# Performance work log

Hardware: AMD Instinct MI355X
Metric: run time of the kernel (lower is better)

## Reference

```python
import jax, jax.numpy as jnp
import numpy as np

B, T, K, FT, FP, N, H, HEADS, C = 8, 5, 20, 384, 3, 128, 64, 8, 2
ALPHA = 0.2
NEG = -9e15


def gru(x, Wi, Wh, bi, bh):
    # x: [M, L, F] -> (full [M, L, Hd], last [M, Hd]); torch nn.GRU cell math
    Hd = Wh.shape[0]
    gx = jnp.einsum('mlf,fg->mlg', x, Wi) + bi  # precompute input projections

    def step(h, gxt):
        gh = h @ Wh + bh
        xr, xz, xn = jnp.split(gxt, 3, axis=-1)
        hr, hz, hn = jnp.split(gh, 3, axis=-1)
        r = jax.nn.sigmoid(xr + hr)
        z = jax.nn.sigmoid(xz + hz)
        n = jnp.tanh(xn + r * hn)
        h = (1. - z) * n + z * h
        return h, h

    h0 = jnp.zeros((x.shape[0], Hd), x.dtype)
    last, full = jax.lax.scan(step, h0, jnp.swapaxes(gx, 0, 1))
    return jnp.swapaxes(full, 0, 1), last


def temporal_attn(full, last):
    # attend over time using the last hidden state as the query
    a = jax.nn.softmax(jnp.einsum('mlh,mh->ml', full, last), axis=-1)
    return jnp.einsum('ml,mlh->mh', a, full)


def gat_forward(s, p, adj, sm1_Wi, sm1_Wh, sm1_bi, sm1_bh,
                sm2_Wi, sm2_Wh, sm2_bi, sm2_bh,
                pr_Wi, pr_Wh, pr_bi, pr_bh,
                Wb, bb, Wx, bx, W1, a1, W2, a2):
    mask = adj > 0  # [N, N]
    # --- SMEncoder: vectorized over (batch, stock, day) ---
    s_ = jnp.transpose(s, (0, 4, 1, 2, 3)).reshape(B * N * T, K, FT)
    f1, l1 = gru(s_, sm1_Wi, sm1_Wh, sm1_bi, sm1_bh)
    cv = temporal_attn(f1, l1).reshape(B * N, T, H)          # intra-day context
    f2, l2 = gru(cv, sm2_Wi, sm2_Wh, sm2_bi, sm2_bh)
    ct = temporal_attn(f2, l2).reshape(B, N, H)              # inter-day context
    # --- PriceEncoder: vectorized over (batch, stock) ---
    p_ = jnp.transpose(p, (0, 3, 1, 2)).reshape(B * N, T, FP)
    f3, l3 = gru(p_, pr_Wi, pr_Wh, pr_bi, pr_bh)
    qt = temporal_attn(f3, l3).reshape(B, N, H)
    # --- bilinear fusion + per-stock linear head (dropout is eval-mode identity) ---
    X = jnp.tanh(jnp.einsum('bni,oij,bnj->bno', ct, Wb, qt) + bb)   # [B, N, H]
    out1 = jnp.tanh(jnp.einsum('bnh,nch->bnc', X, Wx) + bx)          # [B, N, C]
    # --- multi-head GAT layer 1 (concat + LeakyReLU + adj-masked softmax) ---
    Whd = jnp.einsum('bnh,khf->bknf', X, W1)                         # [B, heads, N, H]
    e = jax.nn.leaky_relu(
        jnp.einsum('bknf,kf->bkn', Whd, a1[:, :H])[:, :, :, None]
        + jnp.einsum('bknf,kf->bkn', Whd, a1[:, H:])[:, :, None, :], ALPHA)
    att = jax.nn.softmax(jnp.where(mask, e, NEG), axis=-1)
    Xh = jax.nn.elu(jnp.einsum('bknm,bkmf->bknf', att, Whd))
    X2 = jnp.transpose(Xh, (0, 2, 1, 3)).reshape(B, N, HEADS * H)    # head concat
    # --- GAT layer 2 -> num_classes ---
    Wh2 = X2 @ W2                                                    # [B, N, C]
    e2 = jax.nn.leaky_relu((Wh2 @ a2[:C])[:, :, None]
                           + (Wh2 @ a2[C:])[:, None, :], ALPHA)
    att2 = jax.nn.softmax(jnp.where(mask, e2, NEG), axis=-1)
    Xo = jnp.einsum('bnm,bmc->bnc', att2, Wh2)
    return jnp.transpose(Xo + out1, (0, 2, 1))                       # [B, C, N]


def setup_inputs():
    key = jax.random.key(0)
    ks = jax.random.split(key, 23)
    g = lambda k, sh, sc=0.05: jax.random.normal(k, sh, jnp.float32) * sc
    adj = (jax.random.uniform(ks[2], (N, N)) < 0.3).astype(jnp.float32)
    adj = jnp.maximum(adj, jnp.eye(N, dtype=jnp.float32))
    return {
        's': jax.random.normal(ks[0], (B, T, K, FT, N), jnp.float32),
        'p': jax.random.normal(ks[1], (B, T, FP, N), jnp.float32),
        'adj': adj,
        'sm1_Wi': g(ks[3], (FT, 3 * H)), 'sm1_Wh': g(ks[4], (H, 3 * H)),
        'sm1_bi': g(ks[5], (3 * H,)), 'sm1_bh': g(ks[6], (3 * H,)),
        'sm2_Wi': g(ks[7], (H, 3 * H)), 'sm2_Wh': g(ks[8], (H, 3 * H)),
        'sm2_bi': g(ks[9], (3 * H,)), 'sm2_bh': g(ks[10], (3 * H,)),
        'pr_Wi': g(ks[11], (FP, 3 * H)), 'pr_Wh': g(ks[12], (H, 3 * H)),
        'pr_bi': g(ks[13], (3 * H,)), 'pr_bh': g(ks[14], (3 * H,)),
        'Wb': g(ks[15], (H, H, H)), 'bb': g(ks[16], (H,)),
        'Wx': g(ks[17], (N, C, H)), 'bx': g(ks[18], (N, C)),
        'W1': g(ks[19], (HEADS, H, H)), 'a1': g(ks[20], (HEADS, 2 * H)),
        'W2': g(ks[21], (HEADS * H, C)), 'a2': g(ks[22], (2 * C,)),
    }


def reference(s, p, adj, sm1_Wi, sm1_Wh, sm1_bi, sm1_bh,
              sm2_Wi, sm2_Wh, sm2_bi, sm2_bh,
              pr_Wi, pr_Wh, pr_bi, pr_bh,
              Wb, bb, Wx, bx, W1, a1, W2, a2):
    return gat_forward(s, p, adj, sm1_Wi, sm1_Wh, sm1_bi, sm1_bh,
                       sm2_Wi, sm2_Wh, sm2_bi, sm2_bh,
                       pr_Wi, pr_Wh, pr_bi, pr_bh,
                       Wb, bb, Wx, bx, W1, a1, W2, a2)
```

## Files before the change

### kernel.cpp

```cpp
#include <hip/hip_runtime.h>
#include <hip/hip_bf16.h>
#include <hip/hip_fp16.h>

#define DI __device__ __forceinline__

namespace {

constexpr int G_  = 192;
constexpr int FT_ = 384;

typedef _Float16 f16x8 __attribute__((ext_vector_type(8)));
typedef _Float16 f16x4 __attribute__((ext_vector_type(4)));
typedef float    f32x4 __attribute__((ext_vector_type(4)));

DI float rcpf(float x) { return __builtin_amdgcn_rcpf(x); }
DI float lrelu(float x) { return x > 0.f ? x : 0.2f * x; }
DI float sigmoidf(float x) { return rcpf(1.f + __expf(-x)); }
DI float tanh_fast(float x) { return 1.f - 2.f * rcpf(__expf(2.f * x) + 1.f); }

__global__ __launch_bounds__(256) void k_cvtB(
    const float* __restrict__ Wi, _Float16* __restrict__ Bt) {
  int v = blockIdx.x * 256 + threadIdx.x;
  int g = v / 384, f = v % 384;
  Bt[v] = (_Float16)Wi[f * 192 + g];
}

__global__ __launch_bounds__(256) void k_gx1(
    const float* __restrict__ s, const _Float16* __restrict__ Bt,
    const float* __restrict__ bi, _Float16* __restrict__ gx1) {
  const int slab = blockIdx.x;
  const int b = slab / 100, rem = slab % 100, t = rem / 20, k = rem % 20;
  const float* A = s + (size_t)((b * 5 + t) * 20 + k) * (FT_ * 128);
  __shared__ __align__(16) _Float16 AsL[128 * 40];
  __shared__ __align__(16) _Float16 BsL[192 * 40];
  __shared__ __align__(16) float bisL[192];
  const int tid = threadIdx.x;
  if (tid < 192) bisL[tid] = bi[tid];
  const int w = tid >> 6, l = tid & 63;
  const int lr = l & 15, lk = l >> 4;

  f32x4 acc[12][2];
#pragma unroll
  for (int gt = 0; gt < 12; ++gt)
#pragma unroll
    for (int nt = 0; nt < 2; ++nt) acc[gt][nt] = (f32x4){0.f, 0.f, 0.f, 0.f};

  for (int kc = 0; kc < 12; ++kc) {
    const int f0 = kc * 32;
#pragma unroll
    for (int pass = 0; pass < 2; ++pass) {
      int task = tid + 256 * pass;
      int n = task & 127, oct = task >> 7;
      const float* src = A + (size_t)(f0 + oct * 8) * 128 + n;
      float v[8];
#pragma unroll
      for (int j = 0; j < 8; ++j) v[j] = src[j * 128];
      f16x8 h;
#pragma unroll
      for (int j = 0; j < 8; ++j) h[j] = (_Float16)v[j];
      *(f16x8*)&AsL[n * 40 + oct * 8] = h;
    }
#pragma unroll
    for (int pass = 0; pass < 3; ++pass) {
      int c = tid + 256 * pass;
      int g = c >> 2, oct = c & 3;
      f16x8 h = *(const f16x8*)&Bt[(size_t)g * 384 + f0 + oct * 8];
      *(f16x8*)&BsL[g * 40 + oct * 8] = h;
    }
    __syncthreads();
    f16x8 aN[2];
#pragma unroll
    for (int nt = 0; nt < 2; ++nt)
      aN[nt] = *(const f16x8*)&AsL[(w * 32 + nt * 16 + lr) * 40 + lk * 8];
#pragma unroll
    for (int gt = 0; gt < 12; ++gt) {
      f16x8 bW = *(const f16x8*)&BsL[(gt * 16 + lr) * 40 + lk * 8];
      acc[gt][0] = __builtin_amdgcn_mfma_f32_16x16x32_f16(bW, aN[0], acc[gt][0], 0, 0, 0);
      acc[gt][1] = __builtin_amdgcn_mfma_f32_16x16x32_f16(bW, aN[1], acc[gt][1], 0, 0, 0);
    }
    __syncthreads();
  }
  const size_t base3 = ((size_t)k * 40 + b * 5 + t) * 8;
#pragma unroll
  for (int nt = 0; nt < 2; ++nt) {
    const int ngrp = w * 2 + nt;
    _Float16* dstbase = gx1 + ((base3 + ngrp) * 3) * 1024 + (size_t)l * 16;
#pragma unroll
    for (int gate = 0; gate < 3; ++gate) {
      f16x8 h0, h1;
#pragma unroll
      for (int tq = 0; tq < 4; ++tq) {
        const int gt = gate * 4 + tq;
        f32x4 bias = *(const f32x4*)&bisL[gt * 16 + lk * 4];
        f32x4 c = acc[gt][nt];
#pragma unroll
        for (int r = 0; r < 4; ++r) {
          float v = c[r] + bias[r];
          if (tq < 2) h0[tq * 4 + r] = (_Float16)v;
          else        h1[(tq - 2) * 4 + r] = (_Float16)v;
        }
      }
      *(f16x8*)(dstbase + (size_t)gate * 1024) = h0;
      *(f16x8*)(dstbase + (size_t)gate * 1024 + 8) = h1;
    }
  }
}

__global__ __launch_bounds__(64, 1) void k_scan1m(
    const _Float16* __restrict__ gx, const float* __restrict__ Wh,
    const float* __restrict__ bh, _Float16* __restrict__ cvh) {
  const int wv = blockIdx.x;
  const int b = wv / 40, rem = wv % 40, t = rem / 8, ng = rem % 8;
  const int l = threadIdx.x;
  const int seq = l & 15, rg = l >> 4;

  __shared__ __align__(16) _Float16 histL[20][64][24];
  __shared__ __align__(16) _Float16 red[16][72];

  f16x8 whF[12][2];
#pragma unroll
  for (int gt = 0; gt < 12; ++gt)
#pragma unroll
    for (int c = 0; c < 2; ++c) {
      f16x8 h;
#pragma unroll
      for (int j = 0; j < 8; ++j)
        h[j] = (_Float16)Wh[(size_t)(32 * c + rg * 8 + j) * 192 + gt * 16 + seq];
      whF[gt][c] = h;
    }
  f32x4 bhF[12];
#pragma unroll
  for (int gt = 0; gt < 12; ++gt)
    bhF[gt] = *(const f32x4*)&bh[gt * 16 + rg * 4];

  float h16[16];
#pragma unroll
  for (int j = 0; j < 16; ++j) h16[j] = 0.f;

#define GXP(kk) (gx + ((((size_t)(kk) * 40 + b * 5 + t) * 8 + ng) * 3) * 1024 + (size_t)l * 16)

  f16x8 gxc[3][2], gxn[3][2], gxn2[3][2];
  {
    const _Float16* p0 = GXP(0);
    const _Float16* p1 = GXP(1);
    const _Float16* p2 = GXP(2);
#pragma unroll
    for (int g = 0; g < 3; ++g) {
      gxc[g][0]  = *(const f16x8*)(p0 + g * 1024);
      gxc[g][1]  = *(const f16x8*)(p0 + g * 1024 + 8);
      gxn[g][0]  = *(const f16x8*)(p1 + g * 1024);
      gxn[g][1]  = *(const f16x8*)(p1 + g * 1024 + 8);
      gxn2[g][0] = *(const f16x8*)(p2 + g * 1024);
      gxn2[g][1] = *(const f16x8*)(p2 + g * 1024 + 8);
    }
  }

  f16x8 bf0, bf1;
  f32x4 acc[12];

#define GATES_AND_H(KCONST_HIST)                                               \
  {                                                                            \
    _Float16* hp = &histL[KCONST_HIST][l][0];                                  \
    f16x8 p0, p1;                                                              \
    _Pragma("unroll")                                                          \
    for (int tq = 0; tq < 4; ++tq) {                                           \
      _Pragma("unroll")                                                        \
      for (int r = 0; r < 4; ++r) {                                            \
        const int idx = tq * 4 + r;                                            \
        float xr = (float)gxc[0][idx >> 3][idx & 7];                           \
        float xz = (float)gxc[1][idx >> 3][idx & 7];                           \
        float xn = (float)gxc[2][idx >> 3][idx & 7];                           \
        float hr = acc[tq][r], hz = acc[4 + tq][r], hnv = acc[8 + tq][r];      \
        float rr = sigmoidf(xr + hr);                                          \
        float zz = sigmoidf(xz + hz);                                          \
        float nn = tanh_fast(xn + rr * hnv);                                   \
        float hv = (1.f - zz) * nn + zz * h16[idx];                            \
        h16[idx] = hv;                                                         \
        if (idx < 8) p0[idx] = (_Float16)hv; else p1[idx - 8] = (_Float16)hv;  \
      }                                                                        \
    }                                                                          \
    *(f16x8*)hp = p0;                                                          \
    *(f16x8*)(hp + 8) = p1;                                                    \
  }

#define REDIST()                                                               \
  {                                                                            \
    _Pragma("unroll")                                                          \
    for (int tq = 0; tq < 4; ++tq) {                                           \
      f16x4 q;                                                                 \
      q[0] = (_Float16)h16[tq * 4 + 0]; q[1] = (_Float16)h16[tq * 4 + 1];      \
      q[2] = (_Float16)h16[tq * 4 + 2]; q[3] = (_Float16)h16[tq * 4 + 3];      \
      *(f16x4*)&red[seq][16 * tq + 4 * rg] = q;                                \
    }                                                                          \
    bf0 = *(const f16x8*)&red[seq][8 * rg];                                    \
    bf1 = *(const f16x8*)&red[seq][32 + 8 * rg];                               \
  }

#pragma unroll
  for (int gt = 0; gt < 12; ++gt) acc[gt] = bhF[gt];
  GATES_AND_H(0)
  REDIST()

  for (int k = 1; k < 19; ++k) {
#pragma unroll
    for (int g = 0; g < 3; ++g) {
      gxc[g][0] = gxn[g][0];  gxc[g][1] = gxn[g][1];
      gxn[g][0] = gxn2[g][0]; gxn[g][1] = gxn2[g][1];
    }
    if (k < 18) {
      const _Float16* pn = GXP(k + 2);
#pragma unroll
      for (int g = 0; g < 3; ++g) {
        gxn2[g][0] = *(const f16x8*)(pn + g * 1024);
        gxn2[g][1] = *(const f16x8*)(pn + g * 1024 + 8);
      }
    }
#pragma unroll
    for (int gt = 0; gt < 12; ++gt) {
      acc[gt] = bhF[gt];
      acc[gt] = __builtin_amdgcn_mfma_f32_16x16x32_f16(whF[gt][0], bf0, acc[gt], 0, 0, 0);
      acc[gt] = __builtin_amdgcn_mfma_f32_16x16x32_f16(whF[gt][1], bf1, acc[gt], 0, 0, 0);
    }
    GATES_AND_H(k)
    REDIST()
  }

#pragma unroll
  for (int g = 0; g < 3; ++g) { gxc[g][0] = gxn[g][0]; gxc[g][1] = gxn[g][1]; }
#pragma unroll
  for (int gt = 0; gt < 12; ++gt) {
    acc[gt] = bhF[gt];
    acc[gt] = __builtin_amdgcn_mfma_f32_16x16x32_f16(whF[gt][0], bf0, acc[gt], 0, 0, 0);
    acc[gt] = __builtin_amdgcn_mfma_f32_16x16x32_f16(whF[gt][1], bf1, acc[gt], 0, 0, 0);
  }
  GATES_AND_H(19)

  float d[20];
#pragma unroll
  for (int kk = 0; kk < 20; ++kk) {
    f16x8 a0 = *(const f16x8*)&histL[kk][l][0];
    f16x8 a1 = *(const f16x8*)&histL[kk][l][8];
    float p = 0.f;
#pragma unroll
    for (int j = 0; j < 8; ++j)
      p += (float)a0[j] * h16[j] + (float)a1[j] * h16[8 + j];
    p += __shfl_xor(p, 16);
    p += __shfl_xor(p, 32);
    d[kk] = p;
  }
  float mx = d[0];
#pragma unroll
  for (int kk = 1; kk < 20; ++kk) mx = fmaxf(mx, d[kk]);
  float sum = 0.f;
#pragma unroll
  for (int kk = 0; kk < 20; ++kk) { d[kk] = __expf(d[kk] - mx); sum += d[kk]; }
  const float inv = rcpf(sum);
  float av[16];
#pragma unroll
  for (int j = 0; j < 16; ++j) av[j] = 0.f;
#pragma unroll
  for (int kk = 0; kk < 20; ++kk) {
    f16x8 a0 = *(const f16x8*)&histL[kk][l][0];
    f16x8 a1 = *(const f16x8*)&histL[kk][l][8];
    float wgt = d[kk] * inv;
#pragma unroll
    for (int j = 0; j < 8; ++j) {
      av[j]     += wgt * (float)a0[j];
      av[8 + j] += wgt * (float)a1[j];
    }
  }
  const int n = ng * 16 + seq;
  const size_t seqg = (size_t)b * 128 + n;
  _Float16* dst = cvh + (seqg * 5 + t) * 64;
#pragma unroll
  for (int tq = 0; tq < 4; ++tq) {
    f16x4 q;
    q[0] = (_Float16)av[tq * 4 + 0]; q[1] = (_Float16)av[tq * 4 + 1];
    q[2] = (_Float16)av[tq * 4 + 2]; q[3] = (_Float16)av[tq * 4 + 3];
    *(f16x4*)&dst[16 * tq + 4 * rg] = q;
  }
#undef GXP
#undef GATES_AND_H
#undef REDIST
}

__global__ __launch_bounds__(64, 1) void k_scan2m(
    const _Float16* __restrict__ cvh, const float* __restrict__ Wi,
    const float* __restrict__ Wh, const float* __restrict__ bi,
    const float* __restrict__ bh, float* __restrict__ ct) {
  const int l = threadIdx.x;
  const int seq = l & 15, rg = l >> 4;
  const size_t seqg0 = (size_t)blockIdx.x * 16;

  __shared__ __align__(16) _Float16 histL[5][64][24];
  __shared__ __align__(16) _Float16 red[16][72];

  f16x8 wiF[12][2], whF[12][2];
#pragma unroll
  for (int gt = 0; gt < 12; ++gt)
#pragma unroll
    for (int c = 0; c < 2; ++c) {
      f16x8 hi, hh;
#pragma unroll
      for (int j = 0; j < 8; ++j) {
        hi[j] = (_Float16)Wi[(size_t)(32 * c + rg * 8 + j) * 192 + gt * 16 + seq];
        hh[j] = (_Float16)Wh[(size_t)(32 * c + rg * 8 + j) * 192 + gt * 16 + seq];
      }
      wiF[gt][c] = hi; whF[gt][c] = hh;
    }
  f32x4 biF[12], bhF[12];
#pragma unroll
  for (int gt = 0; gt < 12; ++gt) {
    biF[gt] = *(const f32x4*)&bi[gt * 16 + rg * 4];
    bhF[gt] = *(const f32x4*)&bh[gt * 16 + rg * 4];
  }

  float h16[16];
#pragma unroll
  for (int j = 0; j < 16; ++j) h16[j] = 0.f;
  f16x8 bf0, bf1;

#pragma unroll
  for (int t = 0; t < 5; ++t) {
    const _Float16* xp = cvh + ((seqg0 + seq) * 5 + t) * 64;
    f16x8 xf0 = *(const f16x8*)(xp + 8 * rg);
    f16x8 xf1 = *(const f16x8*)(xp + 32 + 8 * rg);
    f32x4 accX[12], accH[12];
#pragma unroll
    for (int gt = 0; gt < 12; ++gt) {
      accX[gt] = biF[gt];
      accX[gt] = __builtin_amdgcn_mfma_f32_16x16x32_f16(wiF[gt][0], xf0, accX[gt], 0, 0, 0);
      accX[gt] = __builtin_amdgcn_mfma_f32_16x16x32_f16(wiF[gt][1], xf1, accX[gt], 0, 0, 0);
      accH[gt] = bhF[gt];
      if (t > 0) {
        accH[gt] = __builtin_amdgcn_mfma_f32_16x16x32_f16(whF[gt][0], bf0, accH[gt], 0, 0, 0);
        accH[gt] = __builtin_amdgcn_mfma_f32_16x16x32_f16(whF[gt][1], bf1, accH[gt], 0, 0, 0);
      }
    }
    _Float16* hp = &histL[t][l][0];
    f16x8 p0, p1;
#pragma unroll
    for (int tq = 0; tq < 4; ++tq) {
#pragma unroll
      for (int r = 0; r < 4; ++r) {
        const int idx = tq * 4 + r;
        float xr = accX[tq][r], xz = accX[4 + tq][r], xn = accX[8 + tq][r];
        float hr = accH[tq][r], hz = accH[4 + tq][r], hnv = accH[8 + tq][r];
        float rr = sigmoidf(xr + hr);
        float zz = sigmoidf(xz + hz);
        float nn = tanh_fast(xn + rr * hnv);
        float hv = (1.f - zz) * nn + zz * h16[idx];
        h16[idx] = hv;
        if (idx < 8) p0[idx] = (_Float16)hv; else p1[idx - 8] = (_Float16)hv;
      }
    }
    *(f16x8*)hp = p0;
    *(f16x8*)(hp + 8) = p1;
    if (t < 4) {
#pragma unroll
      for (int tq = 0; tq < 4; ++tq) {
        f16x4 q;
        q[0] = (_Float16)h16[tq * 4 + 0]; q[1] = (_Float16)h16[tq * 4 + 1];
        q[2] = (_Float16)h16[tq * 4 + 2]; q[3] = (_Float16)h16[tq * 4 + 3];
        *(f16x4*)&red[seq][16 * tq + 4 * rg] = q;
      }
      bf0 = *(const f16x8*)&red[seq][8 * rg];
      bf1 = *(const f16x8*)&red[seq][32 + 8 * rg];
    }
  }

  float d[5];
#pragma unroll
  for (int kk = 0; kk < 5; ++kk) {
    f16x8 a0 = *(const f16x8*)&histL[kk][l][0];
    f16x8 a1 = *(const f16x8*)&histL[kk][l][8];
    float p = 0.f;
#pragma unroll
    for (int j = 0; j < 8; ++j)
      p += (float)a0[j] * h16[j] + (float)a1[j] * h16[8 + j];
    p += __shfl_xor(p, 16);
    p += __shfl_xor(p, 32);
    d[kk] = p;
  }
  float mx = d[0];
#pragma unroll
  for (int kk = 1; kk < 5; ++kk) mx = fmaxf(mx, d[kk]);
  float sum = 0.f;
#pragma unroll
  for (int kk = 0; kk < 5; ++kk) { d[kk] = __expf(d[kk] - mx); sum += d[kk]; }
  const float inv = rcpf(sum);
  float av[16];
#pragma unroll
  for (int j = 0; j < 16; ++j) av[j] = 0.f;
#pragma unroll
  for (int kk = 0; kk < 5; ++kk) {
    f16x8 a0 = *(const f16x8*)&histL[kk][l][0];
    f16x8 a1 = *(const f16x8*)&histL[kk][l][8];
    float wgt = d[kk] * inv;
#pragma unroll
    for (int j = 0; j < 8; ++j) {
      av[j]     += wgt * (float)a0[j];
      av[8 + j] += wgt * (float)a1[j];
    }
  }
  float* dst = ct + (seqg0 + seq) * 64;
#pragma unroll
  for (int tq = 0; tq < 4; ++tq) {
    float4 o = make_float4(av[tq * 4], av[tq * 4 + 1], av[tq * 4 + 2], av[tq * 4 + 3]);
    *(float4*)&dst[16 * tq + 4 * rg] = o;
  }
}

__global__ __launch_bounds__(192) void k_scan3(
    const float* __restrict__ p, const float* __restrict__ Wi,
    const float* __restrict__ Wh, const float* __restrict__ bi,
    const float* __restrict__ bh, float* __restrict__ outv) {
  const int s0 = blockIdx.x * 4;
  const int tid = threadIdx.x;
  __shared__ __align__(16) float hist[4][5][64];
  __shared__ float xp[4][3];
  __shared__ float ghl[4][192], gxl[4][192];
  __shared__ float dls[4][5], als[4][5];
  float wic[3], whc[64];
#pragma unroll
  for (int f = 0; f < 3; ++f) wic[f] = Wi[f * G_ + tid];
#pragma unroll
  for (int i = 0; i < 64; ++i) whc[i] = Wh[i * G_ + tid];
  const float big = bi[tid], bhg = bh[tid];

  for (int t = 0; t < 5; ++t) {
    if (tid < 12) {
      int ss = tid / 3, f = tid % 3;
      int seq = s0 + ss, b = seq >> 7, n = seq & 127;
      xp[ss][f] = p[((size_t)(b * 5 + t) * 3 + f) * 128 + n];
    }
    __syncthreads();
#pragma unroll
    for (int ss = 0; ss < 4; ++ss) {
      gxl[ss][tid] = xp[ss][0] * wic[0] + xp[ss][1] * wic[1] + xp[ss][2] * wic[2] + big;
      float ah = 0.f;
      if (t > 0) {
        const float4* hq = (const float4*)&hist[ss][t - 1][0];
#pragma unroll
        for (int q = 0; q < 16; ++q) {
          float4 h4 = hq[q];
          ah += h4.x * whc[4 * q]     + h4.y * whc[4 * q + 1]
              + h4.z * whc[4 * q + 2] + h4.w * whc[4 * q + 3];
        }
      }
      ghl[ss][tid] = ah + bhg;
    }
    __syncthreads();
#pragma unroll
    for (int base = 0; base < 256; base += 192) {
      int tk = base + tid;
      if (tk < 256) {
        int ss = tk >> 6, i = tk & 63;
        float xr = gxl[ss][i], xz = gxl[ss][64 + i], xn = gxl[ss][128 + i];
        float hr = ghl[ss][i], hz = ghl[ss][64 + i], hn = ghl[ss][128 + i];
        float r  = sigmoidf(xr + hr);
        float z  = sigmoidf(xz + hz);
        float nn = tanh_fast(xn + r * hn);
        float hp = (t == 0) ? 0.f : hist[ss][t - 1][i];
        hist[ss][t][i] = (1.f - z) * nn + z * hp;
      }
    }
    __syncthreads();
  }
  if (tid < 20) {
    int ss = tid / 5, kk = tid % 5;
    float d = 0.f;
#pragma unroll
    for (int i = 0; i < 64; ++i) d += hist[ss][kk][i] * hist[ss][4][i];
    dls[ss][kk] = d;
  }
  __syncthreads();
  if (tid < 20) {
    int ss = tid / 5, kk = tid % 5;
    float mx = -3.4e38f;
#pragma unroll
    for (int j = 0; j < 5; ++j) mx = fmaxf(mx, dls[ss][j]);
    als[ss][kk] = __expf(dls[ss][kk] - mx);
  }
  __syncthreads();
  for (int idx = tid; idx < 256; idx += 192) {
    int ss = idx >> 6, i = idx & 63;
    float sum = 0.f, a = 0.f;
#pragma unroll
    for (int kk = 0; kk < 5; ++kk) sum += als[ss][kk];
#pragma unroll
    for (int kk = 0; kk < 5; ++kk) a += als[ss][kk] * hist[ss][kk][i];
    outv[(size_t)(s0 + ss) * 64 + i] = a * rcpf(sum);
  }
}

__global__ __launch_bounds__(256) void k_bilinear(
    const float* __restrict__ ct, const float* __restrict__ qt,
    const float* __restrict__ Wb, const float* __restrict__ bb,
    float* __restrict__ X) {
  const int bn0 = blockIdx.x * 4;
  const int tid = threadIdx.x;
  __shared__ float ctl[4][64], qtl[4][64];
  {
    int ss = tid >> 6, i = tid & 63;
    ctl[ss][i] = ct[(size_t)(bn0 + ss) * 64 + i];
    qtl[ss][i] = qt[(size_t)(bn0 + ss) * 64 + i];
  }
  __syncthreads();
  const int o = tid >> 2, part = tid & 3, j0 = part << 4;
  float qr[4][16];
#pragma unroll
  for (int pp = 0; pp < 4; ++pp)
#pragma unroll
    for (int q = 0; q < 16; ++q) qr[pp][q] = qtl[pp][j0 + q];
  float acc[4] = {0.f, 0.f, 0.f, 0.f};
  const float* wb = Wb + (size_t)o * 4096 + j0;
  for (int i = 0; i < 64; ++i) {
    const float4* w4 = (const float4*)(wb + i * 64);
    float tmp[4] = {0.f, 0.f, 0.f, 0.f};
#pragma unroll
    for (int q = 0; q < 4; ++q) {
      float4 w = w4[q];
#pragma unroll
      for (int pp = 0; pp < 4; ++pp)
        tmp[pp] += w.x * qr[pp][4 * q]     + w.y * qr[pp][4 * q + 1]
                 + w.z * qr[pp][4 * q + 2] + w.w * qr[pp][4 * q + 3];
    }
#pragma unroll
    for (int pp = 0; pp < 4; ++pp) acc[pp] += ctl[pp][i] * tmp[pp];
  }
#pragma unroll
  for (int pp = 0; pp < 4; ++pp) {
    acc[pp] += __shfl_xor(acc[pp], 1);
    acc[pp] += __shfl_xor(acc[pp], 2);
  }
  if (part == 0) {
    float bbv = bb[o];
#pragma unroll
    for (int pp = 0; pp < 4; ++pp)
      X[(size_t)(bn0 + pp) * 64 + o] = tanh_fast(acc[pp] + bbv);
  }
}

__global__ __launch_bounds__(256) void k_gat1(
    const float* __restrict__ X, const float* __restrict__ W1,
    const float* __restrict__ a1, const float* __restrict__ adj,
    float* __restrict__ X2) {
  const int bid = blockIdx.x;
  const int b = bid >> 4, k = (bid >> 1) & 7, nh = bid & 1;
  const int tid = threadIdx.x;
  __shared__ __align__(16) float whd[128][68];
  __shared__ float w1l[64][64];
  __shared__ float d1l[128], d2l[128];
  for (int v = tid; v < 4096; v += 256) w1l[v >> 6][v & 63] = W1[(size_t)k * 4096 + v];
  __syncthreads();
  {
    const int f = tid & 63, ng = tid >> 6;
    const float* Xb = X + (size_t)b * 128 * 64;
    for (int n = ng * 32; n < ng * 32 + 32; ++n) {
      float a = 0.f;
#pragma unroll
      for (int h = 0; h < 64; ++h) a += Xb[n * 64 + h] * w1l[h][f];
      whd[n][f] = a;
    }
  }
  __syncthreads();
  if (tid < 128) {
    const int n = tid;
    float da = 0.f, db = 0.f;
#pragma unroll
    for (int f = 0; f < 64; ++f) {
      float w = whd[n][f];
      da += w * a1[k * 128 + f];
      db += w * a1[k * 128 + 64 + f];
    }
    d1l[n] = da; d2l[n] = db;
  }
  __syncthreads();
  {
    const int n = nh * 64 + (tid & 63), fq = tid >> 6, f0 = fq * 16;
    unsigned long long mlo = 0ull, mhi = 0ull;
    for (int m = 0; m < 64; ++m) if (adj[n * 128 + m] > 0.f)      mlo |= (1ull << m);
    for (int m = 0; m < 64; ++m) if (adj[n * 128 + 64 + m] > 0.f) mhi |= (1ull << m);
    const float d1n = d1l[n];
    float mx = -3.4e38f;
    for (int m = 0; m < 128; ++m) {
      bool on = (m < 64) ? (((mlo >> m) & 1ull) != 0) : (((mhi >> (m - 64)) & 1ull) != 0);
      float e = lrelu(d1n + d2l[m]);
      mx = fmaxf(mx, on ? e : -3.4e38f);
    }
    float sum = 0.f;
    float acc[16];
#pragma unroll
    for (int q = 0; q < 16; ++q) acc[q] = 0.f;
    for (int m = 0; m < 128; ++m) {
      bool on = (m < 64) ? (((mlo >> m) & 1ull) != 0) : (((mhi >> (m - 64)) & 1ull) != 0);
      float w = on ? __expf(lrelu(d1n + d2l[m]) - mx) : 0.f;
      sum += w;
      const float4* wr = (const float4*)&whd[m][f0];
#pragma unroll
      for (int q4 = 0; q4 < 4; ++q4) {
        float4 wv = wr[q4];
        acc[4 * q4]     += w * wv.x;
        acc[4 * q4 + 1] += w * wv.y;
        acc[4 * q4 + 2] += w * wv.z;
        acc[4 * q4 + 3] += w * wv.w;
      }
    }
    float inv = rcpf(sum);
    float* dst = X2 + ((size_t)b * 128 + n) * 512 + k * 64 + f0;
#pragma unroll
    for (int q = 0; q < 16; ++q) {
      float v = acc[q] * inv;
      dst[q] = v > 0.f ? v : (__expf(v) - 1.f);
    }
  }
}

__global__ __launch_bounds__(256) void k_wh2(
    const float* __restrict__ X, const float* __restrict__ Wx, const float* __restrict__ bx,
    const float* __restrict__ X2, const float* __restrict__ W2, const float* __restrict__ a2,
    float* __restrict__ out1g, float* __restrict__ wh2g,
    float* __restrict__ d2ag, float* __restrict__ d2bg) {
  const int b = blockIdx.x >> 3, nq = blockIdx.x & 7;
  const int tid = threadIdx.x;
  __shared__ float w2l[1024];
  for (int v = tid; v < 1024; v += 256) w2l[v] = W2[v];
  __syncthreads();
  const int w = tid >> 6, l = tid & 63;
  const float a20 = a2[0], a21 = a2[1], a22 = a2[2], a23 = a2[3];
#pragma unroll
  for (int it = 0; it < 4; ++it) {
    int n = nq * 16 + w * 4 + it;
    int bn = b * 128 + n;
    const float* xr = X2 + (size_t)bn * 512 + l * 8;
    float4 xa = *(const float4*)xr;
    float4 xb = *(const float4*)(xr + 4);
    float xs[8] = {xa.x, xa.y, xa.z, xa.w, xb.x, xb.y, xb.z, xb.w};
    float s0 = 0.f, s1 = 0.f;
#pragma unroll
    for (int j = 0; j < 8; ++j) {
      s0 += xs[j] * w2l[(l * 8 + j) * 2];
      s1 += xs[j] * w2l[(l * 8 + j) * 2 + 1];
    }
#pragma unroll
    for (int d = 1; d < 64; d <<= 1) { s0 += __shfl_xor(s0, d); s1 += __shfl_xor(s1, d); }
    if (l == 0) {
      wh2g[bn * 2] = s0; wh2g[bn * 2 + 1] = s1;
      d2ag[bn] = s0 * a20 + s1 * a21;
      d2bg[bn] = s0 * a22 + s1 * a23;
    }
  }
  if (tid < 32) {
    int n = nq * 16 + (tid >> 1), c = tid & 1;
    int bn = b * 128 + n;
    const float* xrow = X + (size_t)bn * 64;
    float a = 0.f;
#pragma unroll
    for (int h = 0; h < 64; ++h) a += xrow[h] * Wx[(n * 2 + c) * 64 + h];
    out1g[bn * 2 + c] = tanh_fast(a + bx[n * 2 + c]);
  }
}

__global__ __launch_bounds__(128) void k_final(
    const float* __restrict__ adj, const float* __restrict__ wh2g,
    const float* __restrict__ d2ag, const float* __restrict__ d2bg,
    const float* __restrict__ out1g, float* __restrict__ out) {
  const int b = blockIdx.x;
  const int tid = threadIdx.x;
  __shared__ float wh2l[128][2];
  __shared__ float dbl_[128];
  wh2l[tid][0] = wh2g[(size_t)(b * 128 + tid) * 2];
  wh2l[tid][1] = wh2g[(size_t)(b * 128 + tid) * 2 + 1];
  dbl_[tid] = d2bg[b * 128 + tid];
  __syncthreads();
  const int n = tid;
  unsigned long long mlo = 0ull, mhi = 0ull;
  for (int m = 0; m < 64; ++m) if (adj[n * 128 + m] > 0.f)      mlo |= (1ull << m);
  for (int m = 0; m < 64; ++m) if (adj[n * 128 + 64 + m] > 0.f) mhi |= (1ull << m);
  const float dan = d2ag[b * 128 + n];
  float mx = -3.4e38f;
  for (int m = 0; m < 128; ++m) {
    bool on = (m < 64) ? (((mlo >> m) & 1ull) != 0) : (((mhi >> (m - 64)) & 1ull) != 0);
    float e = lrelu(dan + dbl_[m]);
    mx = fmaxf(mx, on ? e : -3.4e38f);
  }
  float sum = 0.f, x0 = 0.f, x1 = 0.f;
  for (int m = 0; m < 128; ++m) {
    bool on = (m < 64) ? (((mlo >> m) & 1ull) != 0) : (((mhi >> (m - 64)) & 1ull) != 0);
    float w = on ? __expf(lrelu(dan + dbl_[m]) - mx) : 0.f;
    sum += w; x0 += w * wh2l[m][0]; x1 += w * wh2l[m][1];
  }
  float inv = rcpf(sum);
  out[(size_t)(b * 2 + 0) * 128 + n] = x0 * inv + out1g[(size_t)(b * 128 + n) * 2];
  out[(size_t)(b * 2 + 1) * 128 + n] = x1 * inv + out1g[(size_t)(b * 128 + n) * 2 + 1];
}

}

extern "C" void kernel_launch(void* const* d_in, const int* in_sizes, int n_in,
                              void* d_out, int out_size, void* d_ws, size_t ws_size,
                              hipStream_t stream) {
  (void)in_sizes; (void)n_in; (void)out_size;
  const float* s      = (const float*)d_in[0];
  const float* p      = (const float*)d_in[1];
  const float* adj    = (const float*)d_in[2];
  const float* sm1_Wi = (const float*)d_in[3];
  const float* sm1_Wh = (const float*)d_in[4];
  const float* sm1_bi = (const float*)d_in[5];
  const float* sm1_bh = (const float*)d_in[6];
  const float* sm2_Wi = (const float*)d_in[7];
  const float* sm2_Wh = (const float*)d_in[8];
  const float* sm2_bi = (const float*)d_in[9];
  const float* sm2_bh = (const float*)d_in[10];
  const float* pr_Wi  = (const float*)d_in[11];
  const float* pr_Wh  = (const float*)d_in[12];
  const float* pr_bi  = (const float*)d_in[13];
  const float* pr_bh  = (const float*)d_in[14];
  const float* Wb     = (const float*)d_in[15];
  const float* bb     = (const float*)d_in[16];
  const float* Wx     = (const float*)d_in[17];
  const float* bx     = (const float*)d_in[18];
  const float* W1     = (const float*)d_in[19];
  const float* a1     = (const float*)d_in[20];
  const float* W2     = (const float*)d_in[21];
  const float* a2     = (const float*)d_in[22];

  if (ws_size < 43540480u) return;
  char* ws = (char*)d_ws;
  _Float16* gx1  = (_Float16*)ws;
  _Float16* cvh  = (_Float16*)(ws + 39321600);
  float* ct      = (float*)(ws + 40632320);
  float* qt      = (float*)(ws + 40894464);
  float* X       = (float*)(ws + 41156608);
  float* X2      = (float*)(ws + 41418752);
  _Float16* Bt   = (_Float16*)(ws + 41418752);
  float* wh2g    = (float*)(ws + 43515904);
  float* out1g   = (float*)(ws + 43524096);
  float* d2ag    = (float*)(ws + 43532288);
  float* d2bg    = (float*)(ws + 43536384);

  hipLaunchKernelGGL(k_cvtB,     dim3(288),  dim3(256), 0, stream, sm1_Wi, Bt);
  hipLaunchKernelGGL(k_gx1,      dim3(800),  dim3(256), 0, stream, s, Bt, sm1_bi, gx1);
  hipLaunchKernelGGL(k_scan1m,   dim3(320),  dim3(64),  0, stream, gx1, sm1_Wh, sm1_bh, cvh);
  hipLaunchKernelGGL(k_scan2m,   dim3(64),   dim3(64),  0, stream, cvh, sm2_Wi, sm2_Wh, sm2_bi, sm2_bh, ct);
  hipLaunchKernelGGL(k_scan3,    dim3(256),  dim3(192), 0, stream, p, pr_Wi, pr_Wh, pr_bi, pr_bh, qt);
  hipLaunchKernelGGL(k_bilinear, dim3(256),  dim3(256), 0, stream, ct, qt, Wb, bb, X);
  hipLaunchKernelGGL(k_gat1,     dim3(128),  dim3(256), 0, stream, X, W1, a1, adj, X2);
  hipLaunchKernelGGL(k_wh2,      dim3(64),   dim3(256), 0, stream, X, Wx, bx, X2, W2, a2, out1g, wh2g, d2ag, d2bg);
  hipLaunchKernelGGL(k_final,    dim3(8),    dim3(128), 0, stream, adj, wh2g, d2ag, d2bg, out1g, (float*)d_out);
}
```

Measured before the change: 476.5 us.

## Merge price GRU into MFMA scan2 kernel and fuse GAT head kernels

The price-encoder GRU now runs inside the scan2 MFMA kernel as an extra 64 blocks, computing its tiny input projection with scalar FMAs from shared memory and its recurrence with the same MFMA path. The separate scalar k_scan3 kernel is removed. The k_wh2 and k_final kernels are merged into one per-batch k_head kernel that keeps intermediates in shared memory, which saves a launch and the global round trips. The trade-off is that the head now uses only 8 blocks for the W2 projection work, so it has less parallelism, and the price GRU now uses fp16 MFMA inputs instead of fp32.

```diff
diff --git a/kernel.cpp b/kernel.cpp
--- a/kernel.cpp
+++ b/kernel.cpp
@@ -284,35 +284,68 @@
 #undef REDIST
 }
 
-__global__ __launch_bounds__(64, 1) void k_scan2m(
-    const _Float16* __restrict__ cvh, const float* __restrict__ Wi,
-    const float* __restrict__ Wh, const float* __restrict__ bi,
-    const float* __restrict__ bh, float* __restrict__ ct) {
+__global__ __launch_bounds__(64, 1) void k_scan23(
+    const _Float16* __restrict__ cvh, const float* __restrict__ Wi2,
+    const float* __restrict__ Wh2w, const float* __restrict__ bi2,
+    const float* __restrict__ bh2, float* __restrict__ ct,
+    const float* __restrict__ p, const float* __restrict__ Wi3,
+    const float* __restrict__ Wh3, const float* __restrict__ bi3,
+    const float* __restrict__ bh3, float* __restrict__ qt) {
   const int l = threadIdx.x;
   const int seq = l & 15, rg = l >> 4;
-  const size_t seqg0 = (size_t)blockIdx.x * 16;
 
   __shared__ __align__(16) _Float16 histL[5][64][24];
   __shared__ __align__(16) _Float16 red[16][72];
-
-  f16x8 wiF[12][2], whF[12][2];
+  __shared__ float wi3L[576];
+  __shared__ float bi3L[192];
+  __shared__ float x3L[240];
+
+  const bool isPrice = blockIdx.x >= 64;
+  const size_t seqg0 = (size_t)(isPrice ? blockIdx.x - 64 : blockIdx.x) * 16;
+  const float* Wh = isPrice ? Wh3 : Wh2w;
+  const float* bh = isPrice ? bh3 : bh2;
+
+  f16x8 whF[12][2];
 #pragma unroll
   for (int gt = 0; gt < 12; ++gt)
 #pragma unroll
     for (int c = 0; c < 2; ++c) {
-      f16x8 hi, hh;
-#pragma unroll
-      for (int j = 0; j < 8; ++j) {
-        hi[j] = (_Float16)Wi[(size_t)(32 * c + rg * 8 + j) * 192 + gt * 16 + seq];
+      f16x8 hh;
+#pragma unroll
+      for (int j = 0; j < 8; ++j)
         hh[j] = (_Float16)Wh[(size_t)(32 * c + rg * 8 + j) * 192 + gt * 16 + seq];
+      whF[gt][c] = hh;
+    }
+  f32x4 bhF[12];
+#pragma unroll
+  for (int gt = 0; gt < 12; ++gt)
+    bhF[gt] = *(const f32x4*)&bh[gt * 16 + rg * 4];
+
+  f16x8 wiF[12][2];
+  f32x4 biF[12];
+  if (!isPrice) {
+#pragma unroll
+    for (int gt = 0; gt < 12; ++gt)
+#pragma unroll
+      for (int c = 0; c < 2; ++c) {
+        f16x8 hi;
+#pragma unroll
+        for (int j = 0; j < 8; ++j)
+          hi[j] = (_Float16)Wi2[(size_t)(32 * c + rg * 8 + j) * 192 + gt * 16 + seq];
+        wiF[gt][c] = hi;
       }
-      wiF[gt][c] = hi; whF[gt][c] = hh;
-    }
-  f32x4 biF[12], bhF[12];
-#pragma unroll
-  for (int gt = 0; gt < 12; ++gt) {
-    biF[gt] = *(const f32x4*)&bi[gt * 16 + rg * 4];
-    bhF[gt] = *(const f32x4*)&bh[gt * 16 + rg * 4];
+#pragma unroll
+    for (int gt = 0; gt < 12; ++gt)
+      biF[gt] = *(const f32x4*)&bi2[gt * 16 + rg * 4];
+  } else {
+    const int b = (int)(seqg0 >> 7), n0 = (int)(seqg0 & 127);
+    for (int idx = l; idx < 576; idx += 64) wi3L[idx] = Wi3[idx];
+    for (int idx = l; idx < 192; idx += 64) bi3L[idx] = bi3[idx];
+    for (int idx = l; idx < 240; idx += 64) {
+      int t = idx / 48, r = idx % 48, f = r / 16, sq = r % 16;
+      x3L[idx] = p[((size_t)(b * 5 + t) * 3 + f) * 128 + n0 + sq];
+    }
+    __syncthreads();
   }
 
   float h16[16];
@@ -322,15 +355,36 @@
 
 #pragma unroll
   for (int t = 0; t < 5; ++t) {
-    const _Float16* xp = cvh + ((seqg0 + seq) * 5 + t) * 64;
-    f16x8 xf0 = *(const f16x8*)(xp + 8 * rg);
-    f16x8 xf1 = *(const f16x8*)(xp + 32 + 8 * rg);
     f32x4 accX[12], accH[12];
+    if (!isPrice) {
+      const _Float16* xp = cvh + ((seqg0 + seq) * 5 + t) * 64;
+      f16x8 xf0 = *(const f16x8*)(xp + 8 * rg);
+      f16x8 xf1 = *(const f16x8*)(xp + 32 + 8 * rg);
+#pragma unroll
+      for (int gt = 0; gt < 12; ++gt) {
+        accX[gt] = biF[gt];
+        accX[gt] = __builtin_amdgcn_mfma_f32_16x16x32_f16(wiF[gt][0], xf0, accX[gt], 0, 0, 0);
+        accX[gt] = __builtin_amdgcn_mfma_f32_16x16x32_f16(wiF[gt][1], xf1, accX[gt], 0, 0, 0);
+      }
+    } else {
+      const float x0 = x3L[t * 48 + seq];
+      const float x1 = x3L[t * 48 + 16 + seq];
+      const float x2 = x3L[t * 48 + 32 + seq];
+#pragma unroll
+      for (int G = 0; G < 3; ++G)
+#pragma unroll
+        for (int tq = 0; tq < 4; ++tq) {
+          f32x4 v;
+#pragma unroll
+          for (int r = 0; r < 4; ++r) {
+            const int g = G * 64 + 16 * tq + 4 * rg + r;
+            v[r] = bi3L[g] + wi3L[g] * x0 + wi3L[192 + g] * x1 + wi3L[384 + g] * x2;
+          }
+          accX[G * 4 + tq] = v;
+        }
+    }
 #pragma unroll
     for (int gt = 0; gt < 12; ++gt) {
-      accX[gt] = biF[gt];
-      accX[gt] = __builtin_amdgcn_mfma_f32_16x16x32_f16(wiF[gt][0], xf0, accX[gt], 0, 0, 0);
-      accX[gt] = __builtin_amdgcn_mfma_f32_16x16x32_f16(wiF[gt][1], xf1, accX[gt], 0, 0, 0);
       accH[gt] = bhF[gt];
       if (t > 0) {
         accH[gt] = __builtin_amdgcn_mfma_f32_16x16x32_f16(whF[gt][0], bf0, accH[gt], 0, 0, 0);
@@ -374,13 +428,13 @@
   for (int kk = 0; kk < 5; ++kk) {
     f16x8 a0 = *(const f16x8*)&histL[kk][l][0];
     f16x8 a1 = *(const f16x8*)&histL[kk][l][8];
-    float p = 0.f;
+    float pq = 0.f;
 #pragma unroll
     for (int j = 0; j < 8; ++j)
-      p += (float)a0[j] * h16[j] + (float)a1[j] * h16[8 + j];
-    p += __shfl_xor(p, 16);
-    p += __shfl_xor(p, 32);
-    d[kk] = p;
+      pq += (float)a0[j] * h16[j] + (float)a1[j] * h16[8 + j];
+    pq += __shfl_xor(pq, 16);
+    pq += __shfl_xor(pq, 32);
+    d[kk] = pq;
   }
   float mx = d[0];
 #pragma unroll
@@ -403,94 +457,11 @@
       av[8 + j] += wgt * (float)a1[j];
     }
   }
-  float* dst = ct + (seqg0 + seq) * 64;
+  float* dst = (isPrice ? qt : ct) + (seqg0 + seq) * 64;
 #pragma unroll
   for (int tq = 0; tq < 4; ++tq) {
     float4 o = make_float4(av[tq * 4], av[tq * 4 + 1], av[tq * 4 + 2], av[tq * 4 + 3]);
     *(float4*)&dst[16 * tq + 4 * rg] = o;
-  }
-}
-
-__global__ __launch_bounds__(192) void k_scan3(
-    const float* __restrict__ p, const float* __restrict__ Wi,
-    const float* __restrict__ Wh, const float* __restrict__ bi,
-    const float* __restrict__ bh, float* __restrict__ outv) {
-  const int s0 = blockIdx.x * 4;
-  const int tid = threadIdx.x;
-  __shared__ __align__(16) float hist[4][5][64];
-  __shared__ float xp[4][3];
-  __shared__ float ghl[4][192], gxl[4][192];
-  __shared__ float dls[4][5], als[4][5];
-  float wic[3], whc[64];
-#pragma unroll
-  for (int f = 0; f < 3; ++f) wic[f] = Wi[f * G_ + tid];
-#pragma unroll
-  for (int i = 0; i < 64; ++i) whc[i] = Wh[i * G_ + tid];
-  const float big = bi[tid], bhg = bh[tid];
-
-  for (int t = 0; t < 5; ++t) {
-    if (tid < 12) {
-      int ss = tid / 3, f = tid % 3;
-      int seq = s0 + ss, b = seq >> 7, n = seq & 127;
-      xp[ss][f] = p[((size_t)(b * 5 + t) * 3 + f) * 128 + n];
-    }
-    __syncthreads();
-#pragma unroll
-    for (int ss = 0; ss < 4; ++ss) {
-      gxl[ss][tid] = xp[ss][0] * wic[0] + xp[ss][1] * wic[1] + xp[ss][2] * wic[2] + big;
-      float ah = 0.f;
-      if (t > 0) {
-        const float4* hq = (const float4*)&hist[ss][t - 1][0];
-#pragma unroll
-        for (int q = 0; q < 16; ++q) {
-          float4 h4 = hq[q];
-          ah += h4.x * whc[4 * q]     + h4.y * whc[4 * q + 1]
-              + h4.z * whc[4 * q + 2] + h4.w * whc[4 * q + 3];
-        }
-      }
-      ghl[ss][tid] = ah + bhg;
-    }
-    __syncthreads();
-#pragma unroll
-    for (int base = 0; base < 256; base += 192) {
-      int tk = base + tid;
-      if (tk < 256) {
-        int ss = tk >> 6, i = tk & 63;
-        float xr = gxl[ss][i], xz = gxl[ss][64 + i], xn = gxl[ss][128 + i];
-        float hr = ghl[ss][i], hz = ghl[ss][64 + i], hn = ghl[ss][128 + i];
-        float r  = sigmoidf(xr + hr);
-        float z  = sigmoidf(xz + hz);
-        float nn = tanh_fast(xn + r * hn);
-        float hp = (t == 0) ? 0.f : hist[ss][t - 1][i];
-        hist[ss][t][i] = (1.f - z) * nn + z * hp;
-      }
-    }
-    __syncthreads();
-  }
-  if (tid < 20) {
-    int ss = tid / 5, kk = tid % 5;
-    float d = 0.f;
-#pragma unroll
-    for (int i = 0; i < 64; ++i) d += hist[ss][kk][i] * hist[ss][4][i];
-    dls[ss][kk] = d;
-  }
-  __syncthreads();
-  if (tid < 20) {
-    int ss = tid / 5, kk = tid % 5;
-    float mx = -3.4e38f;
-#pragma unroll
-    for (int j = 0; j < 5; ++j) mx = fmaxf(mx, dls[ss][j]);
-    als[ss][kk] = __expf(dls[ss][kk] - mx);
-  }
-  __syncthreads();
-  for (int idx = tid; idx < 256; idx += 192) {
-    int ss = idx >> 6, i = idx & 63;
-    float sum = 0.f, a = 0.f;
-#pragma unroll
-    for (int kk = 0; kk < 5; ++kk) sum += als[ss][kk];
-#pragma unroll
-    for (int kk = 0; kk < 5; ++kk) a += als[ss][kk] * hist[ss][kk][i];
-    outv[(size_t)(s0 + ss) * 64 + i] = a * rcpf(sum);
   }
 }
 
@@ -617,23 +588,23 @@
   }
 }
 
-__global__ __launch_bounds__(256) void k_wh2(
+__global__ __launch_bounds__(256) void k_head(
     const float* __restrict__ X, const float* __restrict__ Wx, const float* __restrict__ bx,
     const float* __restrict__ X2, const float* __restrict__ W2, const float* __restrict__ a2,
-    float* __restrict__ out1g, float* __restrict__ wh2g,
-    float* __restrict__ d2ag, float* __restrict__ d2bg) {
-  const int b = blockIdx.x >> 3, nq = blockIdx.x & 7;
+    const float* __restrict__ adj, float* __restrict__ out) {
+  const int b = blockIdx.x;
   const int tid = threadIdx.x;
   __shared__ float w2l[1024];
+  __shared__ float wh2l[128][2];
+  __shared__ float d2aL[128], d2bL[128];
+  __shared__ float out1L[128][2];
   for (int v = tid; v < 1024; v += 256) w2l[v] = W2[v];
   __syncthreads();
   const int w = tid >> 6, l = tid & 63;
   const float a20 = a2[0], a21 = a2[1], a22 = a2[2], a23 = a2[3];
-#pragma unroll
-  for (int it = 0; it < 4; ++it) {
-    int n = nq * 16 + w * 4 + it;
-    int bn = b * 128 + n;
-    const float* xr = X2 + (size_t)bn * 512 + l * 8;
+  for (int it = 0; it < 32; ++it) {
+    int n = w * 32 + it;
+    const float* xr = X2 + ((size_t)b * 128 + n) * 512 + l * 8;
     float4 xa = *(const float4*)xr;
     float4 xb = *(const float4*)(xr + 4);
     float xs[8] = {xa.x, xa.y, xa.z, xa.w, xb.x, xb.y, xb.z, xb.w};
@@ -646,54 +617,45 @@
 #pragma unroll
     for (int d = 1; d < 64; d <<= 1) { s0 += __shfl_xor(s0, d); s1 += __shfl_xor(s1, d); }
     if (l == 0) {
-      wh2g[bn * 2] = s0; wh2g[bn * 2 + 1] = s1;
-      d2ag[bn] = s0 * a20 + s1 * a21;
-      d2bg[bn] = s0 * a22 + s1 * a23;
-    }
-  }
-  if (tid < 32) {
-    int n = nq * 16 + (tid >> 1), c = tid & 1;
-    int bn = b * 128 + n;
-    const float* xrow = X + (size_t)bn * 64;
-    float a = 0.f;
-#pragma unroll
-    for (int h = 0; h < 64; ++h) a += xrow[h] * Wx[(n * 2 + c) * 64 + h];
-    out1g[bn * 2 + c] = tanh_fast(a + bx[n * 2 + c]);
-  }
-}
-
-__global__ __launch_bounds__(128) void k_final(
-    const float* __restrict__ adj, const float* __restrict__ wh2g,
-    const float* __restrict__ d2ag, const float* __restrict__ d2bg,
-    const float* __restrict__ out1g, float* __restrict__ out) {
-  const int b = blockIdx.x;
-  const int tid = threadIdx.x;
-  __shared__ float wh2l[128][2];
-  __shared__ float dbl_[128];
-  wh2l[tid][0] = wh2g[(size_t)(b * 128 + tid) * 2];
-  wh2l[tid][1] = wh2g[(size_t)(b * 128 + tid) * 2 + 1];
-  dbl_[tid] = d2bg[b * 128 + tid];
+      wh2l[n][0] = s0; wh2l[n][1] = s1;
+      d2aL[n] = s0 * a20 + s1 * a21;
+      d2bL[n] = s0 * a22 + s1 * a23;
+    }
+  }
+  if (tid < 128) {
+    int n = tid;
+    const float* xrow = X + ((size_t)b * 128 + n) * 64;
+#pragma unroll
+    for (int c = 0; c < 2; ++c) {
+      float a = 0.f;
+#pragma unroll
+      for (int h = 0; h < 64; ++h) a += xrow[h] * Wx[(n * 2 + c) * 64 + h];
+      out1L[n][c] = tanh_fast(a + bx[n * 2 + c]);
+    }
+  }
   __syncthreads();
-  const int n = tid;
-  unsigned long long mlo = 0ull, mhi = 0ull;
-  for (int m = 0; m < 64; ++m) if (adj[n * 128 + m] > 0.f)      mlo |= (1ull << m);
-  for (int m = 0; m < 64; ++m) if (adj[n * 128 + 64 + m] > 0.f) mhi |= (1ull << m);
-  const float dan = d2ag[b * 128 + n];
-  float mx = -3.4e38f;
-  for (int m = 0; m < 128; ++m) {
-    bool on = (m < 64) ? (((mlo >> m) & 1ull) != 0) : (((mhi >> (m - 64)) & 1ull) != 0);
-    float e = lrelu(dan + dbl_[m]);
-    mx = fmaxf(mx, on ? e : -3.4e38f);
-  }
-  float sum = 0.f, x0 = 0.f, x1 = 0.f;
-  for (int m = 0; m < 128; ++m) {
-    bool on = (m < 64) ? (((mlo >> m) & 1ull) != 0) : (((mhi >> (m - 64)) & 1ull) != 0);
-    float w = on ? __expf(lrelu(dan + dbl_[m]) - mx) : 0.f;
-    sum += w; x0 += w * wh2l[m][0]; x1 += w * wh2l[m][1];
-  }
-  float inv = rcpf(sum);
-  out[(size_t)(b * 2 + 0) * 128 + n] = x0 * inv + out1g[(size_t)(b * 128 + n) * 2];
-  out[(size_t)(b * 2 + 1) * 128 + n] = x1 * inv + out1g[(size_t)(b * 128 + n) * 2 + 1];
+  if (tid < 128) {
+    const int n = tid;
+    unsigned long long mlo = 0ull, mhi = 0ull;
+    for (int m = 0; m < 64; ++m) if (adj[n * 128 + m] > 0.f)      mlo |= (1ull << m);
+    for (int m = 0; m < 64; ++m) if (adj[n * 128 + 64 + m] > 0.f) mhi |= (1ull << m);
+    const float dan = d2aL[n];
+    float mx = -3.4e38f;
+    for (int m = 0; m < 128; ++m) {
+      bool on = (m < 64) ? (((mlo >> m) & 1ull) != 0) : (((mhi >> (m - 64)) & 1ull) != 0);
+      float e = lrelu(dan + d2bL[m]);
+      mx = fmaxf(mx, on ? e : -3.4e38f);
+    }
+    float sum = 0.f, x0 = 0.f, x1 = 0.f;
+    for (int m = 0; m < 128; ++m) {
+      bool on = (m < 64) ? (((mlo >> m) & 1ull) != 0) : (((mhi >> (m - 64)) & 1ull) != 0);
+      float wgt = on ? __expf(lrelu(dan + d2bL[m]) - mx) : 0.f;
+      sum += wgt; x0 += wgt * wh2l[m][0]; x1 += wgt * wh2l[m][1];
+    }
+    float inv = rcpf(sum);
+    out[(size_t)(b * 2 + 0) * 128 + n] = x0 * inv + out1L[n][0];
+    out[(size_t)(b * 2 + 1) * 128 + n] = x1 * inv + out1L[n][1];
+  }
 }
 
 }
@@ -735,18 +697,14 @@
   float* X       = (float*)(ws + 41156608);
   float* X2      = (float*)(ws + 41418752);
   _Float16* Bt   = (_Float16*)(ws + 41418752);
-  float* wh2g    = (float*)(ws + 43515904);
-  float* out1g   = (float*)(ws + 43524096);
-  float* d2ag    = (float*)(ws + 43532288);
-  float* d2bg    = (float*)(ws + 43536384);
 
   hipLaunchKernelGGL(k_cvtB,     dim3(288),  dim3(256), 0, stream, sm1_Wi, Bt);
   hipLaunchKernelGGL(k_gx1,      dim3(800),  dim3(256), 0, stream, s, Bt, sm1_bi, gx1);
   hipLaunchKernelGGL(k_scan1m,   dim3(320),  dim3(64),  0, stream, gx1, sm1_Wh, sm1_bh, cvh);
-  hipLaunchKernelGGL(k_scan2m,   dim3(64),   dim3(64),  0, stream, cvh, sm2_Wi, sm2_Wh, sm2_bi, sm2_bh, ct);
-  hipLaunchKernelGGL(k_scan3,    dim3(256),  dim3(192), 0, stream, p, pr_Wi, pr_Wh, pr_bi, pr_bh, qt);
+  hipLaunchKernelGGL(k_scan23,   dim3(128),  dim3(64),  0, stream,
+                     cvh, sm2_Wi, sm2_Wh, sm2_bi, sm2_bh, ct,
+                     p, pr_Wi, pr_Wh, pr_bi, pr_bh, qt);
   hipLaunchKernelGGL(k_bilinear, dim3(256),  dim3(256), 0, stream, ct, qt, Wb, bb, X);
   hipLaunchKernelGGL(k_gat1,     dim3(128),  dim3(256), 0, stream, X, W1, a1, adj, X2);
-  hipLaunchKernelGGL(k_wh2,      dim3(64),   dim3(256), 0, stream, X, Wx, bx, X2, W2, a2, out1g, wh2g, d2ag, d2bg);
-  hipLaunchKernelGGL(k_final,    dim3(8),    dim3(128), 0, stream, adj, wh2g, d2ag, d2bg, out1g, (float*)d_out);
-}
+  hipLaunchKernelGGL(k_head,     dim3(8),    dim3(256), 0, stream, X, Wx, bx, X2, W2, a2, adj, (float*)d_out);
+}
```

Result: no change. 469.2 us (-1.5%).
